# Kernel tuning notes

Hardware: AMD Instinct MI355X
Metric: run time of the kernel (lower is better)

## Reference

```python
import jax, jax.numpy as jnp
import numpy as np

B, IN, OUT = 8192, 4096, 2048  # OUT must equal 32*64 per betta/gamma sizes


def setup_inputs() -> dict:
    key = jax.random.key(0)
    kx, kw = jax.random.split(key, 2)
    X = jax.random.normal(kx, (B, IN), dtype=jnp.float32)
    # xavier-uniform-like init for W
    limit = float(np.sqrt(6.0 / (IN + OUT)))
    W = jax.random.uniform(kw, (IN, OUT), minval=-limit, maxval=limit, dtype=jnp.float32)
    absmean = jnp.abs(W).mean(axis=0)
    alpha = jnp.abs(W).mean()          # scalar, >= 0
    betta = absmean[:32]               # (32,), >= 0
    gamma = absmean[32:96]             # (64,), >= 0
    return {"X": X, "W": W, "alpha": alpha, "betta": betta, "gamma": gamma}


def reference(X, W, alpha, betta, gamma):
    # module applies relu_ to alpha/betta/gamma data before the functional call
    alpha = jax.nn.relu(alpha)
    betta = jax.nn.relu(betta)
    gamma = jax.nn.relu(gamma)
    X_bin = jnp.sign(X)                # (B, IN)
    W_bin = jnp.sign(W)                # (IN, OUT)
    # scale[i*64+j] = alpha * betta[i] * gamma[j] -> (OUT,)
    scale = (alpha * jnp.outer(betta, gamma)).reshape(-1)
    return (X_bin @ W_bin) * scale     # (B, OUT)
```

## Files before the change

kernel.cpp:

```cpp
#include <hip/hip_runtime.h>


#define M_DIM 8192
#define K_DIM 4096
#define N_DIM 2048
#define NTK   (K_DIM / 128)
#define PANEL (128 * 128 * 16)
#define KSTEP 8192
#define BUFB  24576

typedef int i32x4 __attribute__((ext_vector_type(4)));
typedef int i32x8 __attribute__((ext_vector_type(8)));
typedef float f32x16 __attribute__((ext_vector_type(16)));

__device__ __forceinline__ unsigned int nib4(float x) {
  unsigned int s = (__float_as_uint(x) >> 28) & 0x8u;
  return x == 0.0f ? 0u : (0x2u | s);
}

__device__ __forceinline__ unsigned int pack8(const float* f) {
  unsigned int p = 0;
#pragma unroll
  for (int j = 0; j < 8; ++j) p |= nib4(f[j]) << (4 * j);
  return p;
}

__device__ __forceinline__ void gload_lds16(const void* g, void* lds) {
  __builtin_amdgcn_global_load_lds(
      (const __attribute__((address_space(1))) unsigned int*)g,
      (__attribute__((address_space(3))) unsigned int*)lds, 16, 0, 0);
}

__global__ __launch_bounds__(256) void binX_kernel(
    const float* __restrict__ X, unsigned char* __restrict__ Xq) {
  __shared__ float tile[32][260];
  const int t = threadIdx.x;
  const int rg = blockIdx.x >> 4;
  const int kc = blockIdx.x & 15;
  const int lrow = t >> 6;
  const int col4 = (t & 63) * 4;
#pragma unroll
  for (int i = 0; i < 8; ++i)
    *(float4*)&tile[i * 4 + lrow][col4] =
        *(const float4*)&X[(size_t)(rg * 32 + i * 4 + lrow) * K_DIM + kc * 256 + col4];
  __syncthreads();
  const int s = t >> 5;
  const int r = t & 31;
  float f[32];
#pragma unroll
  for (int q = 0; q < 8; ++q)
    *(float4*)&f[q * 4] = *(const float4*)&tile[r][s * 32 + q * 4];
  uint4 gq;
  gq.x = pack8(f + 0);  gq.y = pack8(f + 8);
  gq.z = pack8(f + 16); gq.w = pack8(f + 24);
  const int row = rg * 32 + r;
  const int kslot = kc * 8 + s;
  unsigned char* dst = Xq + (size_t)(row >> 7) * PANEL +
                       ((size_t)kslot * 128 + (row & 127)) * 16;
  *(uint4*)dst = gq;
}

__global__ __launch_bounds__(256) void binW_kernel(
    const float* __restrict__ W, unsigned char* __restrict__ Wq) {
  __shared__ float tile[32][260];
  const int t = threadIdx.x;
  const int q = blockIdx.x >> 7;
  const int kt = (blockIdx.x >> 3) & 15;
  const int s = blockIdx.x & 7;
#pragma unroll
  for (int i = 0; i < 8; ++i) {
    int row = i * 4 + (t >> 6);
    int col4 = (t & 63) * 4;
    *(float4*)&tile[row][col4] =
        *(const float4*)&W[(size_t)(kt * 256 + s * 32 + row) * N_DIM + q * 256 + col4];
  }
  __syncthreads();
  float f[32];
#pragma unroll
  for (int k = 0; k < 32; ++k) f[k] = tile[k][t];
  uint4 gq;
  gq.x = pack8(f + 0);  gq.y = pack8(f + 8);
  gq.z = pack8(f + 16); gq.w = pack8(f + 24);
  const int n = q * 256 + t;
  const int kslot = kt * 8 + s;
  unsigned char* dst = Wq + (size_t)(n >> 7) * PANEL +
                       ((size_t)kslot * 128 + (n & 127)) * 16;
  *(uint4*)dst = gq;
}

__global__ __launch_bounds__(256, 2) void gemm_fp4_kernel(
    const unsigned char* __restrict__ Aq,
    const unsigned char* __restrict__ Bq,
    const float* __restrict__ alpha,
    const float* __restrict__ betta,
    const float* __restrict__ gamma,
    float* __restrict__ C) {
  __shared__ __align__(16) unsigned char smem[3 * BUFB];

  const int t = threadIdx.x;
  const int lane = t & 63;
  const int l31 = lane & 31;
  const int lhi = lane >> 5;
  const int w = t >> 6;
  const int wr = w >> 1;
  const int wc = w & 1;

  const int bid = blockIdx.x;
  const int j = bid >> 3;
  const int bm = (bid & 7) * 4 + (j & 3);
  const int bn = j >> 2;
  const int row0 = bm * 256;
  const int col0 = bn * 128;

  const unsigned char* Asrc0 = Aq + (size_t)(2 * bm) * PANEL;
  const unsigned char* Asrc1 = Asrc0 + PANEL;
  const unsigned char* Bsrc  = Bq + (size_t)bn * PANEL;

  f32x16 acc[4][2];
#pragma unroll
  for (int fm = 0; fm < 4; ++fm)
#pragma unroll
    for (int fn = 0; fn < 2; ++fn)
#pragma unroll
      for (int r = 0; r < 16; ++r) acc[fm][fn][r] = 0.f;

  i32x8 a8[4], b8[2];
#pragma unroll
  for (int i = 0; i < 4; ++i)
#pragma unroll
    for (int e = 0; e < 8; ++e) a8[i][e] = 0;
#pragma unroll
  for (int i = 0; i < 2; ++i)
#pragma unroll
    for (int e = 0; e < 8; ++e) b8[i][e] = 0;

  auto stage = [&](int kt, unsigned char* buf) {
    const unsigned char* a0 = Asrc0 + kt * KSTEP;
    const unsigned char* a1 = Asrc1 + kt * KSTEP;
    const unsigned char* b  = Bsrc  + kt * KSTEP;
#pragma unroll
    for (int p = 0; p < 2; ++p) {
      const int c = p * 256 + t;
      gload_lds16(a0 + c * 16, buf + c * 16);
      gload_lds16(a1 + c * 16, buf + 8192 + c * 16);
      gload_lds16(b  + c * 16, buf + 16384 + c * 16);
    }
  };

  auto compute = [&](const unsigned char* buf) {
    const unsigned char* pA = buf + wr * 8192;
    const unsigned char* pB = buf + 16384;
#pragma unroll
    for (int kk = 0; kk < 2; ++kk) {
      const int g = kk * 2 + lhi;
#pragma unroll
      for (int fm = 0; fm < 4; ++fm)
        *(i32x4*)&a8[fm] = *(const i32x4*)&pA[(g * 128 + fm * 32 + l31) * 16];
#pragma unroll
      for (int fn = 0; fn < 2; ++fn)
        *(i32x4*)&b8[fn] = *(const i32x4*)&pB[(g * 128 + wc * 64 + fn * 32 + l31) * 16];
      __builtin_amdgcn_s_setprio(1);
#pragma unroll
      for (int fm = 0; fm < 4; ++fm)
#pragma unroll
        for (int fn = 0; fn < 2; ++fn)
          acc[fm][fn] = __builtin_amdgcn_mfma_scale_f32_32x32x64_f8f6f4(
              a8[fm], b8[fn], acc[fm][fn], 4, 4,
              0, 0x7F7F7F7F, 0, 0x7F7F7F7F);
      __builtin_amdgcn_s_setprio(0);
    }
  };

  unsigned char* P0 = smem;
  unsigned char* P1 = smem + BUFB;
  unsigned char* P2 = smem + 2 * BUFB;

  stage(0, P0);
  stage(1, P1);

  for (int kt = 0; kt < NTK - 1; ++kt) {
    asm volatile("s_waitcnt vmcnt(6)" ::: "memory");
    __builtin_amdgcn_s_barrier();
    __builtin_amdgcn_sched_barrier(0);
    if (kt + 2 < NTK) stage(kt + 2, P2);
    compute(P0);
    unsigned char* tmp = P0; P0 = P1; P1 = P2; P2 = tmp;
  }
  asm volatile("s_waitcnt vmcnt(0)" ::: "memory");
  __builtin_amdgcn_s_barrier();
  __builtin_amdgcn_sched_barrier(0);
  compute(P0);

  const float ra = fmaxf(alpha[0], 0.0f);
#pragma unroll
  for (int fn = 0; fn < 2; ++fn) {
    const int col = col0 + wc * 64 + fn * 32 + l31;
    const float sc = ra * fmaxf(betta[col >> 6], 0.0f) * fmaxf(gamma[col & 63], 0.0f);
#pragma unroll
    for (int fm = 0; fm < 4; ++fm) {
      const int rbase = row0 + wr * 128 + fm * 32 + 4 * lhi;
#pragma unroll
      for (int r = 0; r < 16; ++r) {
        const int row = rbase + (r & 3) + 8 * (r >> 2);
        C[(size_t)row * N_DIM + col] = acc[fm][fn][r] * sc;
      }
    }
  }
}

extern "C" void kernel_launch(void* const* d_in, const int* in_sizes, int n_in,
                              void* d_out, int out_size, void* d_ws, size_t ws_size,
                              hipStream_t stream) {
  const float* X = (const float*)d_in[0];
  const float* W = (const float*)d_in[1];
  const float* alpha = (const float*)d_in[2];
  const float* betta = (const float*)d_in[3];
  const float* gamma = (const float*)d_in[4];
  float* out = (float*)d_out;

  unsigned char* Xq = (unsigned char*)d_ws;
  unsigned char* Wq = Xq + (size_t)(M_DIM / 128) * PANEL;

  binW_kernel<<<1024, 256, 0, stream>>>(W, Wq);
  binX_kernel<<<4096, 256, 0, stream>>>(X, Xq);
  gemm_fp4_kernel<<<(M_DIM / 256) * (N_DIM / 128), 256, 0, stream>>>(
      Xq, Wq, alpha, betta, gamma, out);
}
```

Before: 72.82 us.

## Fuse binarize kernels and enlarge GEMM tile to 256x256 with 512 threads

Merges the X and W binarization kernels into one launch, removing a kernel boundary. The GEMM block tile grows from 256x128 to 256x256 with 8 waves, so each staged A panel is reused across twice as many columns and the grid halves. Output stores become nontemporal to avoid polluting cache. Larger LDS buffers (96KB for triple buffering) and 512-thread blocks with launch_bounds(512,2) may limit occupancy or strain registers.

```diff
diff --git a/kernel.cpp b/kernel.cpp
--- a/kernel.cpp
+++ b/kernel.cpp
@@ -7,7 +7,7 @@
 #define NTK   (K_DIM / 128)
 #define PANEL (128 * 128 * 16)
 #define KSTEP 8192
-#define BUFB  24576
+#define BUFB  32768
 
 typedef int i32x4 __attribute__((ext_vector_type(4)));
 typedef int i32x8 __attribute__((ext_vector_type(8)));
@@ -31,64 +31,65 @@
       (__attribute__((address_space(3))) unsigned int*)lds, 16, 0, 0);
 }
 
-__global__ __launch_bounds__(256) void binX_kernel(
-    const float* __restrict__ X, unsigned char* __restrict__ Xq) {
+__global__ __launch_bounds__(256) void binXW_kernel(
+    const float* __restrict__ X, const float* __restrict__ W,
+    unsigned char* __restrict__ Xq, unsigned char* __restrict__ Wq) {
   __shared__ float tile[32][260];
   const int t = threadIdx.x;
-  const int rg = blockIdx.x >> 4;
-  const int kc = blockIdx.x & 15;
-  const int lrow = t >> 6;
-  const int col4 = (t & 63) * 4;
-#pragma unroll
-  for (int i = 0; i < 8; ++i)
-    *(float4*)&tile[i * 4 + lrow][col4] =
-        *(const float4*)&X[(size_t)(rg * 32 + i * 4 + lrow) * K_DIM + kc * 256 + col4];
-  __syncthreads();
-  const int s = t >> 5;
-  const int r = t & 31;
-  float f[32];
-#pragma unroll
-  for (int q = 0; q < 8; ++q)
-    *(float4*)&f[q * 4] = *(const float4*)&tile[r][s * 32 + q * 4];
-  uint4 gq;
-  gq.x = pack8(f + 0);  gq.y = pack8(f + 8);
-  gq.z = pack8(f + 16); gq.w = pack8(f + 24);
-  const int row = rg * 32 + r;
-  const int kslot = kc * 8 + s;
-  unsigned char* dst = Xq + (size_t)(row >> 7) * PANEL +
-                       ((size_t)kslot * 128 + (row & 127)) * 16;
-  *(uint4*)dst = gq;
-}
-
-__global__ __launch_bounds__(256) void binW_kernel(
-    const float* __restrict__ W, unsigned char* __restrict__ Wq) {
-  __shared__ float tile[32][260];
-  const int t = threadIdx.x;
-  const int q = blockIdx.x >> 7;
-  const int kt = (blockIdx.x >> 3) & 15;
-  const int s = blockIdx.x & 7;
-#pragma unroll
-  for (int i = 0; i < 8; ++i) {
-    int row = i * 4 + (t >> 6);
-    int col4 = (t & 63) * 4;
-    *(float4*)&tile[row][col4] =
-        *(const float4*)&W[(size_t)(kt * 256 + s * 32 + row) * N_DIM + q * 256 + col4];
+  const int bid = blockIdx.x;
+
+  if (bid < 4096) {
+    const int rg = bid >> 4;
+    const int kc = bid & 15;
+    const int lrow = t >> 6;
+    const int col4 = (t & 63) * 4;
+#pragma unroll
+    for (int i = 0; i < 8; ++i)
+      *(float4*)&tile[i * 4 + lrow][col4] =
+          *(const float4*)&X[(size_t)(rg * 32 + i * 4 + lrow) * K_DIM + kc * 256 + col4];
+    __syncthreads();
+    const int s = t >> 5;
+    const int r = t & 31;
+    float f[32];
+#pragma unroll
+    for (int q = 0; q < 8; ++q)
+      *(float4*)&f[q * 4] = *(const float4*)&tile[r][s * 32 + q * 4];
+    uint4 gq;
+    gq.x = pack8(f + 0);  gq.y = pack8(f + 8);
+    gq.z = pack8(f + 16); gq.w = pack8(f + 24);
+    const int row = rg * 32 + r;
+    const int kslot = kc * 8 + s;
+    unsigned char* dst = Xq + (size_t)(row >> 7) * PANEL +
+                         ((size_t)kslot * 128 + (row & 127)) * 16;
+    *(uint4*)dst = gq;
+  } else {
+    const int idx = bid - 4096;
+    const int q = idx >> 7;
+    const int kt = (idx >> 3) & 15;
+    const int s = idx & 7;
+#pragma unroll
+    for (int i = 0; i < 8; ++i) {
+      int row = i * 4 + (t >> 6);
+      int col4 = (t & 63) * 4;
+      *(float4*)&tile[row][col4] =
+          *(const float4*)&W[(size_t)(kt * 256 + s * 32 + row) * N_DIM + q * 256 + col4];
+    }
+    __syncthreads();
+    float f[32];
+#pragma unroll
+    for (int k = 0; k < 32; ++k) f[k] = tile[k][t];
+    uint4 gq;
+    gq.x = pack8(f + 0);  gq.y = pack8(f + 8);
+    gq.z = pack8(f + 16); gq.w = pack8(f + 24);
+    const int n = q * 256 + t;
+    const int kslot = kt * 8 + s;
+    unsigned char* dst = Wq + (size_t)(n >> 7) * PANEL +
+                         ((size_t)kslot * 128 + (n & 127)) * 16;
+    *(uint4*)dst = gq;
   }
-  __syncthreads();
-  float f[32];
-#pragma unroll
-  for (int k = 0; k < 32; ++k) f[k] = tile[k][t];
-  uint4 gq;
-  gq.x = pack8(f + 0);  gq.y = pack8(f + 8);
-  gq.z = pack8(f + 16); gq.w = pack8(f + 24);
-  const int n = q * 256 + t;
-  const int kslot = kt * 8 + s;
-  unsigned char* dst = Wq + (size_t)(n >> 7) * PANEL +
-                       ((size_t)kslot * 128 + (n & 127)) * 16;
-  *(uint4*)dst = gq;
-}
-
-__global__ __launch_bounds__(256, 2) void gemm_fp4_kernel(
+}
+
+__global__ __launch_bounds__(512, 2) void gemm_fp4_kernel(
     const unsigned char* __restrict__ Aq,
     const unsigned char* __restrict__ Bq,
     const float* __restrict__ alpha,
@@ -102,19 +103,20 @@
   const int l31 = lane & 31;
   const int lhi = lane >> 5;
   const int w = t >> 6;
-  const int wr = w >> 1;
-  const int wc = w & 1;
+  const int wr = w >> 2;
+  const int wc = w & 3;
 
   const int bid = blockIdx.x;
   const int j = bid >> 3;
   const int bm = (bid & 7) * 4 + (j & 3);
   const int bn = j >> 2;
   const int row0 = bm * 256;
-  const int col0 = bn * 128;
+  const int col0 = bn * 256;
 
   const unsigned char* Asrc0 = Aq + (size_t)(2 * bm) * PANEL;
   const unsigned char* Asrc1 = Asrc0 + PANEL;
-  const unsigned char* Bsrc  = Bq + (size_t)bn * PANEL;
+  const unsigned char* Bsrc0 = Bq + (size_t)(2 * bn) * PANEL;
+  const unsigned char* Bsrc1 = Bsrc0 + PANEL;
 
   f32x16 acc[4][2];
 #pragma unroll
@@ -135,21 +137,17 @@
     for (int e = 0; e < 8; ++e) b8[i][e] = 0;
 
   auto stage = [&](int kt, unsigned char* buf) {
-    const unsigned char* a0 = Asrc0 + kt * KSTEP;
-    const unsigned char* a1 = Asrc1 + kt * KSTEP;
-    const unsigned char* b  = Bsrc  + kt * KSTEP;
-#pragma unroll
-    for (int p = 0; p < 2; ++p) {
-      const int c = p * 256 + t;
-      gload_lds16(a0 + c * 16, buf + c * 16);
-      gload_lds16(a1 + c * 16, buf + 8192 + c * 16);
-      gload_lds16(b  + c * 16, buf + 16384 + c * 16);
-    }
+    const size_t ko = (size_t)kt * KSTEP;
+    gload_lds16(Asrc0 + ko + t * 16, buf + t * 16);
+    gload_lds16(Asrc1 + ko + t * 16, buf + 8192 + t * 16);
+    gload_lds16(Bsrc0 + ko + t * 16, buf + 16384 + t * 16);
+    gload_lds16(Bsrc1 + ko + t * 16, buf + 24576 + t * 16);
   };
 
   auto compute = [&](const unsigned char* buf) {
     const unsigned char* pA = buf + wr * 8192;
-    const unsigned char* pB = buf + 16384;
+    const unsigned char* pB = buf + 16384 + (wc >> 1) * 8192;
+    const int cb = (wc & 1) * 64;
 #pragma unroll
     for (int kk = 0; kk < 2; ++kk) {
       const int g = kk * 2 + lhi;
@@ -158,7 +156,7 @@
         *(i32x4*)&a8[fm] = *(const i32x4*)&pA[(g * 128 + fm * 32 + l31) * 16];
 #pragma unroll
       for (int fn = 0; fn < 2; ++fn)
-        *(i32x4*)&b8[fn] = *(const i32x4*)&pB[(g * 128 + wc * 64 + fn * 32 + l31) * 16];
+        *(i32x4*)&b8[fn] = *(const i32x4*)&pB[(g * 128 + cb + fn * 32 + l31) * 16];
       __builtin_amdgcn_s_setprio(1);
 #pragma unroll
       for (int fm = 0; fm < 4; ++fm)
@@ -179,7 +177,7 @@
   stage(1, P1);
 
   for (int kt = 0; kt < NTK - 1; ++kt) {
-    asm volatile("s_waitcnt vmcnt(6)" ::: "memory");
+    asm volatile("s_waitcnt vmcnt(4)" ::: "memory");
     __builtin_amdgcn_s_barrier();
     __builtin_amdgcn_sched_barrier(0);
     if (kt + 2 < NTK) stage(kt + 2, P2);
@@ -202,7 +200,8 @@
 #pragma unroll
       for (int r = 0; r < 16; ++r) {
         const int row = rbase + (r & 3) + 8 * (r >> 2);
-        C[(size_t)row * N_DIM + col] = acc[fm][fn][r] * sc;
+        __builtin_nontemporal_store(acc[fm][fn][r] * sc,
+                                    &C[(size_t)row * N_DIM + col]);
       }
     }
   }
@@ -221,8 +220,7 @@
   unsigned char* Xq = (unsigned char*)d_ws;
   unsigned char* Wq = Xq + (size_t)(M_DIM / 128) * PANEL;
 
-  binW_kernel<<<1024, 256, 0, stream>>>(W, Wq);
-  binX_kernel<<<4096, 256, 0, stream>>>(X, Xq);
-  gemm_fp4_kernel<<<(M_DIM / 256) * (N_DIM / 128), 256, 0, stream>>>(
+  binXW_kernel<<<5120, 256, 0, stream>>>(X, W, Xq, Wq);
+  gemm_fp4_kernel<<<(M_DIM / 256) * (N_DIM / 256), 512, 0, stream>>>(
       Xq, Wq, alpha, betta, gamma, out);
 }
```

Measured after the change: 70.98 us. -2.5%, faster.
